# Performance work log

Hardware: AMD Instinct MI355X
Metric: run time of the kernel (lower is better)

Reference implementation:

```python
import jax, jax.numpy as jnp
import numpy as np

B, S, D, H = 2, 2048, 1024, 16
DK = D // H

def setup_inputs() -> dict:
    key = jax.random.key(0)
    ks = jax.random.split(key, 12)
    def lin(k, shape, fan_in):
        bound = 1.0 / np.sqrt(fan_in)
        return jax.random.uniform(k, shape, jnp.float32, -bound, bound)
    inp = {
        'Q': jax.random.normal(ks[0], (B, S, D), jnp.float32),
        'K': jax.random.normal(ks[1], (B, S, D), jnp.float32),
        'V': jax.random.normal(ks[2], (B, S, D), jnp.float32),
        # padding mask: last 128 key positions of batch element 0 are padding
        'padding_mask': jnp.ones((B, 1, 1, S), jnp.int32).at[0, :, :, -128:].set(0),
        # causal look-ahead mask
        'look_ahead_mask': jnp.tril(jnp.ones((S, S), jnp.int32))[None, None],
        'Wq': lin(ks[3], (D, D), D), 'bq': lin(ks[4], (D,), D),
        'Wk': lin(ks[5], (D, D), D), 'bk': lin(ks[6], (D,), D),
        'Wv': lin(ks[7], (D, D), D), 'bv': lin(ks[8], (D,), D),
        'Wo': lin(ks[9], (D, D), D), 'bo': lin(ks[10], (D,), D),
    }
    return inp

def _split_heads(x):
    # [B,S,D] -> [B,H,S,DK]
    b, s, _ = x.shape
    return x.reshape(b, s, H, DK).transpose(0, 2, 1, 3)

def reference(Q, K, V, padding_mask, look_ahead_mask, Wq, bq, Wk, bk, Wv, bv, Wo, bo):
    q = _split_heads(Q @ Wq.T + bq)  # [B,H,S,DK]
    k = _split_heads(K @ Wk.T + bk)
    v = _split_heads(V @ Wv.T + bv)
    scores = jnp.einsum('bhqd,bhkd->bhqk', q, k) / np.sqrt(DK).astype(np.float32)
    neg_inf = jnp.float32(-jnp.inf)
    scores = jnp.where(padding_mask == 0, neg_inf, scores)
    scores = jnp.where(look_ahead_mask == 0, neg_inf, scores)
    weights = jax.nn.softmax(scores, axis=-1)  # dropout is identity in eval mode
    x = jnp.einsum('bhqk,bhkd->bhqd', weights, v)  # [B,H,S,DK]
    x = x.transpose(0, 2, 1, 3).reshape(Q.shape[0], Q.shape[1], D)
    return x @ Wo.T + bo
```

## Files before the change

kernel.cpp:

```cpp
#include <hip/hip_runtime.h>
#include <hip/hip_bf16.h>

#define B_   2
#define S_   2048
#define D_   1024
#define H_   16
#define DK_  64

typedef unsigned short u16;
typedef __attribute__((ext_vector_type(8))) short bf16x8;
typedef __attribute__((ext_vector_type(4))) float f32x4;

#define QSCALE   0.18033688011112042f
#define SMBIAS  -8.656170245333781f

static __device__ __forceinline__ u16 f2bf(float f) {
  union { float f; unsigned u; } v; v.f = f;
  unsigned r = v.u + 0x7FFF + ((v.u >> 16) & 1);
  return (u16)(r >> 16);
}

static __device__ __forceinline__ void gl_lds16(const void* g, void* l) {
  __builtin_amdgcn_global_load_lds(
      (const __attribute__((address_space(1))) void*)g,
      (__attribute__((address_space(3))) void*)l, 16, 0, 0);
}

__global__ void cvt3(const float4* __restrict__ a, const float4* __restrict__ b, const float4* __restrict__ c,
                     ushort4* __restrict__ oa, ushort4* __restrict__ ob, ushort4* __restrict__ oc, int n4) {
  int y = blockIdx.y;
  const float4* in = (y == 0) ? a : (y == 1) ? b : c;
  ushort4* out = (y == 0) ? oa : (y == 1) ? ob : oc;
  int i = blockIdx.x * blockDim.x + threadIdx.x;
  if (i < n4) {
    float4 v = in[i];
    ushort4 r;
    r.x = f2bf(v.x); r.y = f2bf(v.y); r.z = f2bf(v.z); r.w = f2bf(v.w);
    out[i] = r;
  }
}
__global__ void cvt4(const float4* __restrict__ a, const float4* __restrict__ b, const float4* __restrict__ c,
                     const float4* __restrict__ d, ushort4* __restrict__ oa, ushort4* __restrict__ ob,
                     ushort4* __restrict__ oc, ushort4* __restrict__ od, int n4) {
  int y = blockIdx.y;
  const float4* in = (y == 0) ? a : (y == 1) ? b : (y == 2) ? c : d;
  ushort4* out = (y == 0) ? oa : (y == 1) ? ob : (y == 2) ? oc : od;
  int i = blockIdx.x * blockDim.x + threadIdx.x;
  if (i < n4) {
    float4 v = in[i];
    ushort4 r;
    r.x = f2bf(v.x); r.y = f2bf(v.y); r.z = f2bf(v.z); r.w = f2bf(v.w);
    out[i] = r;
  }
}

__launch_bounds__(256, 2)
__global__ void gemm_qkv(const u16* __restrict__ Xq, const u16* __restrict__ Xk, const u16* __restrict__ Xv,
                         const u16* __restrict__ Wq, const u16* __restrict__ Wk, const u16* __restrict__ Wv,
                         const float* __restrict__ bq, const float* __restrict__ bk, const float* __restrict__ bv,
                         u16* __restrict__ outq, u16* __restrict__ outk, u16* __restrict__ outv) {
  const int z = blockIdx.z;
  const u16* Am; const u16* Bm; int m0, n0;
  if (z == 2) { Am = Wv; Bm = Xv; m0 = blockIdx.x * 128; n0 = blockIdx.y * 128; }
  else if (z == 1) { Am = Xk; Bm = Wk; m0 = blockIdx.y * 128; n0 = blockIdx.x * 128; }
  else { Am = Xq; Bm = Wq; m0 = blockIdx.y * 128; n0 = blockIdx.x * 128; }
  const float* bias = (z == 0) ? bq : (z == 1) ? bk : bv;

  __shared__ __align__(16) u16 As[2][128 * 32];
  __shared__ __align__(16) u16 Bs[2][128 * 32];

  const int tid = threadIdx.x, lane = tid & 63, w = tid >> 6;
  const int q = lane >> 4, cl = lane & 15;
  const int wr = w >> 1, wc = w & 1;

#pragma unroll
  for (int i = 0; i < 2; ++i) {
    int cb = (i * 4 + w) * 64;
    int ch = cb + lane;
    int row = ch >> 2, ko = (ch & 3) << 3;
    gl_lds16(Am + (size_t)(m0 + row) * D_ + ko, As[0] + cb * 8);
    gl_lds16(Bm + (size_t)(n0 + row) * D_ + ko, Bs[0] + cb * 8);
  }

  f32x4 acc[4][4] = {};

  for (int it = 0; it < 32; ++it) {
    const int buf = it & 1;
    __syncthreads();

    if (it < 31) {
      const int k0 = (it + 1) * 32;
#pragma unroll
      for (int i = 0; i < 2; ++i) {
        int cb = (i * 4 + w) * 64;
        int ch = cb + lane;
        int row = ch >> 2, ko = (ch & 3) << 3;
        gl_lds16(Am + (size_t)(m0 + row) * D_ + k0 + ko, As[buf ^ 1] + cb * 8);
        gl_lds16(Bm + (size_t)(n0 + row) * D_ + k0 + ko, Bs[buf ^ 1] + cb * 8);
      }
    }

    const u16* At = As[buf];
    const u16* Bt = Bs[buf];
    bf16x8 af[4], bfr[4];
#pragma unroll
    for (int r = 0; r < 4; ++r) af[r]  = *(const bf16x8*)(At + (wr * 64 + r * 16 + cl) * 32 + q * 8);
#pragma unroll
    for (int c = 0; c < 4; ++c) bfr[c] = *(const bf16x8*)(Bt + (wc * 64 + c * 16 + cl) * 32 + q * 8);
#pragma unroll
    for (int r = 0; r < 4; ++r)
#pragma unroll
      for (int c = 0; c < 4; ++c)
        acc[r][c] = __builtin_amdgcn_mfma_f32_16x16x32_bf16(af[r], bfr[c], acc[r][c], 0, 0, 0);
  }

  if (z == 2) {
#pragma unroll
    for (int r = 0; r < 4; ++r) {
#pragma unroll
      for (int rr = 0; rr < 4; ++rr) {
        int j = m0 + wr * 64 + r * 16 + q * 4 + rr;
        float bval = bias[j];
        int hh = j >> 6, dk = j & 63;
#pragma unroll
        for (int c = 0; c < 4; ++c) {
          int n = n0 + wc * 64 + c * 16 + cl;
          int bb = n >> 11, s = n & (S_ - 1);
          outv[((size_t)(bb * H_ + hh) * DK_ + dk) * S_ + s] = f2bf(acc[r][c][rr] + bval);
        }
      }
    }
  } else {
    const float scale = (z == 0) ? QSCALE : 1.0f;
    u16* o = (z == 0) ? outq : outk;
#pragma unroll
    for (int c = 0; c < 4; ++c) {
      int j = n0 + wc * 64 + c * 16 + cl;
      float bval = bias[j];
      int hh = j >> 6, dk = j & 63;
#pragma unroll
      for (int r = 0; r < 4; ++r) {
#pragma unroll
        for (int rr = 0; rr < 4; ++rr) {
          int n = m0 + wr * 64 + r * 16 + q * 4 + rr;
          int bb = n >> 11, s = n & (S_ - 1);
          o[((size_t)(bb * H_ + hh) * S_ + s) * DK_ + dk] = f2bf((acc[r][c][rr] + bval) * scale);
        }
      }
    }
  }
}

__launch_bounds__(256, 2)
__global__ void attn(const u16* __restrict__ qh, const u16* __restrict__ kh,
                     const u16* __restrict__ vt, const int* __restrict__ pad,
                     u16* __restrict__ attn_out) {
  __shared__ __align__(16) u16 Ks[2][64 * 64];
  __shared__ __align__(16) u16 Vs[2][64 * 64];
  __shared__ __align__(16) u16 Ps[4][16 * 72];

  const int tid = threadIdx.x, lane = tid & 63, w = tid >> 6;
  const int q = lane >> 4, cl = lane & 15;
  const int qt = (int)gridDim.x - 1 - (int)blockIdx.x;
  const int qb = qt * 64, h = blockIdx.y, b = blockIdx.z;

  const u16* Q = qh + (size_t)(b * H_ + h) * S_ * DK_;
  const u16* K = kh + (size_t)(b * H_ + h) * S_ * DK_;
  const u16* V = vt + (size_t)(b * H_ + h) * DK_ * S_;
  const int* pm = pad + b * S_;

  const int qr0 = qb + w * 16;
  bf16x8 qf0 = *(const bf16x8*)(Q + (qr0 + cl) * DK_ + q * 8);
  bf16x8 qf1 = *(const bf16x8*)(Q + (qr0 + cl) * DK_ + 32 + q * 8);

  f32x4 o[4] = {};
  float ls[4] = {0.f, 0.f, 0.f, 0.f};
  u16* Pw = Ps[w];

  const int nkv = qt + 1;

#pragma unroll
  for (int i = 0; i < 2; ++i) {
    int s = (i * 4 + w) * 64 + lane;
    int row = s >> 3;
    int c = (s & 7) ^ (row & 7);
    gl_lds16(K + (size_t)row * DK_ + (c << 3), Ks[0] + (size_t)s * 8);
    gl_lds16(V + (size_t)row * S_ + (c << 3), Vs[0] + (size_t)s * 8);
  }

  for (int it = 0; it < nkv; ++it) {
    const int kb = it << 6;
    const int buf = it & 1;
    __syncthreads();

    if (it + 1 < nkv) {
      const int kb2 = (it + 1) << 6;
#pragma unroll
      for (int i = 0; i < 2; ++i) {
        int s = (i * 4 + w) * 64 + lane;
        int row = s >> 3;
        int c = (s & 7) ^ (row & 7);
        gl_lds16(K + (size_t)(kb2 + row) * DK_ + (c << 3), Ks[buf ^ 1] + (size_t)s * 8);
        gl_lds16(V + (size_t)row * S_ + kb2 + (c << 3), Vs[buf ^ 1] + (size_t)s * 8);
      }
    }

    const u16* Kt = Ks[buf];
    const u16* Vt = Vs[buf];

    bf16x8 kf[4][2];
#pragma unroll
    for (int ct = 0; ct < 4; ++ct) {
      int rk = ct * 16 + cl;
      int c0 = q ^ (rk & 7);
      kf[ct][0] = *(const bf16x8*)(Kt + rk * 64 + (c0 << 3));
      kf[ct][1] = *(const bf16x8*)(Kt + rk * 64 + ((c0 ^ 4) << 3));
    }

    float kbv[4];
#pragma unroll
    for (int ct = 0; ct < 4; ++ct)
      kbv[ct] = (pm[kb + ct * 16 + cl] != 0) ? SMBIAS : -3e38f;

    f32x4 sa[4];
#pragma unroll
    for (int ct = 0; ct < 4; ++ct) {
      f32x4 zz = {};
      zz = __builtin_amdgcn_mfma_f32_16x16x32_bf16(qf0, kf[ct][0], zz, 0, 0, 0);
      zz = __builtin_amdgcn_mfma_f32_16x16x32_bf16(qf1, kf[ct][1], zz, 0, 0, 0);
      sa[ct] = zz;
    }

    if (it < qt) {
#pragma unroll
      for (int ct = 0; ct < 4; ++ct)
#pragma unroll
        for (int rr = 0; rr < 4; ++rr) {
          float p = exp2f(sa[ct][rr] + kbv[ct]);
          ls[rr] += p;
          Pw[(q * 4 + rr) * 72 + ct * 16 + cl] = f2bf(p);
        }
    } else {
#pragma unroll
      for (int ct = 0; ct < 4; ++ct) {
        int kg = kb + ct * 16 + cl;
#pragma unroll
        for (int rr = 0; rr < 4; ++rr) {
          int qg = qr0 + q * 4 + rr;
          float p = (kg <= qg) ? exp2f(sa[ct][rr] + kbv[ct]) : 0.f;
          ls[rr] += p;
          Pw[(q * 4 + rr) * 72 + ct * 16 + cl] = f2bf(p);
        }
      }
    }

    bf16x8 pf0 = *(const bf16x8*)(Pw + cl * 72 + q * 8);
    bf16x8 pf1 = *(const bf16x8*)(Pw + cl * 72 + 32 + q * 8);

#pragma unroll
    for (int ct = 0; ct < 4; ++ct) {
      int rv = ct * 16 + cl;
      int c0 = q ^ (rv & 7);
      bf16x8 vf0 = *(const bf16x8*)(Vt + rv * 64 + (c0 << 3));
      bf16x8 vf1 = *(const bf16x8*)(Vt + rv * 64 + ((c0 ^ 4) << 3));
      o[ct] = __builtin_amdgcn_mfma_f32_16x16x32_bf16(pf0, vf0, o[ct], 0, 0, 0);
      o[ct] = __builtin_amdgcn_mfma_f32_16x16x32_bf16(pf1, vf1, o[ct], 0, 0, 0);
    }
  }

#pragma unroll
  for (int rr = 0; rr < 4; ++rr) {
    float l = ls[rr];
    l += __shfl_xor(l, 1, 64);
    l += __shfl_xor(l, 2, 64);
    l += __shfl_xor(l, 4, 64);
    l += __shfl_xor(l, 8, 64);
    float inv = 1.0f / l;
    int qg = qr0 + q * 4 + rr;
    size_t base = (size_t)(b * S_ + qg) * D_ + h * DK_;
#pragma unroll
    for (int ct = 0; ct < 4; ++ct)
      attn_out[base + ct * 16 + cl] = f2bf(o[ct][rr] * inv);
  }
}

__launch_bounds__(256, 2)
__global__ void gemm_out(const u16* __restrict__ A, const u16* __restrict__ W,
                         const float* __restrict__ bias, float* __restrict__ out) {
  __shared__ __align__(16) u16 As[2][128 * 32];
  __shared__ __align__(16) u16 Bs[2][64 * 32];

  const int tid = threadIdx.x, lane = tid & 63, w = tid >> 6;
  const int q = lane >> 4, cl = lane & 15;
  const int m0 = blockIdx.y * 128, n0 = blockIdx.x * 64;

#pragma unroll
  for (int i = 0; i < 2; ++i) {
    int cb = (i * 4 + w) * 64;
    int ch = cb + lane;
    int row = ch >> 2, ko = (ch & 3) << 3;
    gl_lds16(A + (size_t)(m0 + row) * D_ + ko, As[0] + cb * 8);
  }
  {
    int cb = w * 64;
    int ch = cb + lane;
    int row = ch >> 2, ko = (ch & 3) << 3;
    gl_lds16(W + (size_t)(n0 + row) * D_ + ko, Bs[0] + cb * 8);
  }

  f32x4 acc[2][4] = {};

  for (int it = 0; it < 32; ++it) {
    const int buf = it & 1;
    __syncthreads();

    if (it < 31) {
      const int k0 = (it + 1) * 32;
#pragma unroll
      for (int i = 0; i < 2; ++i) {
        int cb = (i * 4 + w) * 64;
        int ch = cb + lane;
        int row = ch >> 2, ko = (ch & 3) << 3;
        gl_lds16(A + (size_t)(m0 + row) * D_ + k0 + ko, As[buf ^ 1] + cb * 8);
      }
      {
        int cb = w * 64;
        int ch = cb + lane;
        int row = ch >> 2, ko = (ch & 3) << 3;
        gl_lds16(W + (size_t)(n0 + row) * D_ + k0 + ko, Bs[buf ^ 1] + cb * 8);
      }
    }

    const u16* At = As[buf];
    const u16* Bt = Bs[buf];
    bf16x8 af[2], bfr[4];
#pragma unroll
    for (int r = 0; r < 2; ++r) af[r]  = *(const bf16x8*)(At + (w * 32 + r * 16 + cl) * 32 + q * 8);
#pragma unroll
    for (int c = 0; c < 4; ++c) bfr[c] = *(const bf16x8*)(Bt + (c * 16 + cl) * 32 + q * 8);
#pragma unroll
    for (int r = 0; r < 2; ++r)
#pragma unroll
      for (int c = 0; c < 4; ++c)
        acc[r][c] = __builtin_amdgcn_mfma_f32_16x16x32_bf16(af[r], bfr[c], acc[r][c], 0, 0, 0);
  }

#pragma unroll
  for (int c = 0; c < 4; ++c) {
    int j = n0 + c * 16 + cl;
    float bval = bias[j];
#pragma unroll
    for (int r = 0; r < 2; ++r) {
#pragma unroll
      for (int rr = 0; rr < 4; ++rr) {
        int n = m0 + w * 32 + r * 16 + q * 4 + rr;
        out[(size_t)n * D_ + j] = acc[r][c][rr] + bval;
      }
    }
  }
}

extern "C" void kernel_launch(void* const* d_in, const int* in_sizes, int n_in,
                              void* d_out, int out_size, void* d_ws, size_t ws_size,
                              hipStream_t stream) {
  const float* Qf  = (const float*)d_in[0];
  const float* Kf  = (const float*)d_in[1];
  const float* Vf  = (const float*)d_in[2];
  const int*   pad = (const int*)d_in[3];
  const float* Wqf = (const float*)d_in[5];
  const float* bq  = (const float*)d_in[6];
  const float* Wkf = (const float*)d_in[7];
  const float* bk  = (const float*)d_in[8];
  const float* Wvf = (const float*)d_in[9];
  const float* bv  = (const float*)d_in[10];
  const float* Wof = (const float*)d_in[11];
  const float* bo  = (const float*)d_in[12];

  const size_t BSD = (size_t)B_ * S_ * D_;
  const size_t DD  = (size_t)D_ * D_;

  char* ws = (char*)d_ws;
  u16* Qb   = (u16*)ws; ws += BSD * 2;
  u16* Kb   = (u16*)ws; ws += BSD * 2;
  u16* Vb   = (u16*)ws; ws += BSD * 2;
  u16* Wqb  = (u16*)ws; ws += DD * 2;
  u16* Wkb  = (u16*)ws; ws += DD * 2;
  u16* Wvb  = (u16*)ws; ws += DD * 2;
  u16* Wob  = (u16*)ws; ws += DD * 2;
  u16* qhd  = (u16*)ws; ws += BSD * 2;
  u16* khd  = (u16*)ws; ws += BSD * 2;
  u16* vtd  = (u16*)ws; ws += BSD * 2;
  u16* attn_o = (u16*)ws; ws += BSD * 2;

  const int n4 = (int)(BSD / 4);
  const int w4 = (int)(DD / 4);
  dim3 gc3(n4 / 256, 3), gc4(w4 / 256, 4);
  cvt3<<<gc3, 256, 0, stream>>>((const float4*)Qf, (const float4*)Kf, (const float4*)Vf,
                                (ushort4*)Qb, (ushort4*)Kb, (ushort4*)Vb, n4);
  cvt4<<<gc4, 256, 0, stream>>>((const float4*)Wqf, (const float4*)Wkf, (const float4*)Wvf, (const float4*)Wof,
                                (ushort4*)Wqb, (ushort4*)Wkb, (ushort4*)Wvb, (ushort4*)Wob, w4);

  dim3 g1(D_ / 128, (B_ * S_) / 128, 3);
  gemm_qkv<<<g1, 256, 0, stream>>>(Qb, Kb, Vb, Wqb, Wkb, Wvb, bq, bk, bv, qhd, khd, vtd);

  dim3 g2(S_ / 64, H_, B_);
  attn<<<g2, 256, 0, stream>>>(qhd, khd, vtd, pad, attn_o);

  dim3 g3(D_ / 64, (B_ * S_) / 128);
  gemm_out<<<g3, 256, 0, stream>>>(attn_o, Wob, bo, (float*)d_out);
}
```

Baseline: 288.6 us.

## Load attention K/V fragments directly from global memory and merge conversion kernels

The attention kernel no longer stages K and V tiles through double-buffered LDS with async global-to-LDS copies and block barriers. Each wave now reads its K and V MFMA fragments straight from global memory, relying on L2/L1 caching, and interleaves the score MFMAs with the softmax per column tile. Launch bounds are raised to 4 blocks per SIMD to hide the added global latency with occupancy. The two fp32-to-bf16 conversion kernels are merged into one launch, which over-provisions blocks for the small weight matrices. The trade is that each of the four waves in a block now fetches the same K/V tile separately, so the kernel becomes more dependent on cache hit rates.

Result: slower. 420.9 us (+45.8%).

```diff
diff --git a/kernel.cpp b/kernel.cpp
--- a/kernel.cpp
+++ b/kernel.cpp
@@ -26,27 +26,27 @@
       (__attribute__((address_space(3))) void*)l, 16, 0, 0);
 }
 
-__global__ void cvt3(const float4* __restrict__ a, const float4* __restrict__ b, const float4* __restrict__ c,
-                     ushort4* __restrict__ oa, ushort4* __restrict__ ob, ushort4* __restrict__ oc, int n4) {
+__global__ void cvt_all(const float4* __restrict__ s0, const float4* __restrict__ s1,
+                        const float4* __restrict__ s2, const float4* __restrict__ s3,
+                        const float4* __restrict__ s4, const float4* __restrict__ s5,
+                        const float4* __restrict__ s6,
+                        ushort4* __restrict__ d0, ushort4* __restrict__ d1,
+                        ushort4* __restrict__ d2, ushort4* __restrict__ d3,
+                        ushort4* __restrict__ d4, ushort4* __restrict__ d5,
+                        ushort4* __restrict__ d6, int nbig, int nsmall) {
   int y = blockIdx.y;
-  const float4* in = (y == 0) ? a : (y == 1) ? b : c;
-  ushort4* out = (y == 0) ? oa : (y == 1) ? ob : oc;
+  const float4* in; ushort4* out; int n;
+  switch (y) {
+    case 0: in = s0; out = d0; n = nbig; break;
+    case 1: in = s1; out = d1; n = nbig; break;
+    case 2: in = s2; out = d2; n = nbig; break;
+    case 3: in = s3; out = d3; n = nsmall; break;
+    case 4: in = s4; out = d4; n = nsmall; break;
+    case 5: in = s5; out = d5; n = nsmall; break;
+    default: in = s6; out = d6; n = nsmall; break;
+  }
   int i = blockIdx.x * blockDim.x + threadIdx.x;
-  if (i < n4) {
-    float4 v = in[i];
-    ushort4 r;
-    r.x = f2bf(v.x); r.y = f2bf(v.y); r.z = f2bf(v.z); r.w = f2bf(v.w);
-    out[i] = r;
-  }
-}
-__global__ void cvt4(const float4* __restrict__ a, const float4* __restrict__ b, const float4* __restrict__ c,
-                     const float4* __restrict__ d, ushort4* __restrict__ oa, ushort4* __restrict__ ob,
-                     ushort4* __restrict__ oc, ushort4* __restrict__ od, int n4) {
-  int y = blockIdx.y;
-  const float4* in = (y == 0) ? a : (y == 1) ? b : (y == 2) ? c : d;
-  ushort4* out = (y == 0) ? oa : (y == 1) ? ob : (y == 2) ? oc : od;
-  int i = blockIdx.x * blockDim.x + threadIdx.x;
-  if (i < n4) {
+  if (i < n) {
     float4 v = in[i];
     ushort4 r;
     r.x = f2bf(v.x); r.y = f2bf(v.y); r.z = f2bf(v.z); r.w = f2bf(v.w);
@@ -151,12 +151,10 @@
   }
 }
 
-__launch_bounds__(256, 2)
+__launch_bounds__(256, 4)
 __global__ void attn(const u16* __restrict__ qh, const u16* __restrict__ kh,
                      const u16* __restrict__ vt, const int* __restrict__ pad,
                      u16* __restrict__ attn_out) {
-  __shared__ __align__(16) u16 Ks[2][64 * 64];
-  __shared__ __align__(16) u16 Vs[2][64 * 64];
   __shared__ __align__(16) u16 Ps[4][16 * 72];
 
   const int tid = threadIdx.x, lane = tid & 63, w = tid >> 6;
@@ -178,43 +176,15 @@
   u16* Pw = Ps[w];
 
   const int nkv = qt + 1;
-
-#pragma unroll
-  for (int i = 0; i < 2; ++i) {
-    int s = (i * 4 + w) * 64 + lane;
-    int row = s >> 3;
-    int c = (s & 7) ^ (row & 7);
-    gl_lds16(K + (size_t)row * DK_ + (c << 3), Ks[0] + (size_t)s * 8);
-    gl_lds16(V + (size_t)row * S_ + (c << 3), Vs[0] + (size_t)s * 8);
-  }
-
   for (int it = 0; it < nkv; ++it) {
     const int kb = it << 6;
-    const int buf = it & 1;
-    __syncthreads();
-
-    if (it + 1 < nkv) {
-      const int kb2 = (it + 1) << 6;
-#pragma unroll
-      for (int i = 0; i < 2; ++i) {
-        int s = (i * 4 + w) * 64 + lane;
-        int row = s >> 3;
-        int c = (s & 7) ^ (row & 7);
-        gl_lds16(K + (size_t)(kb2 + row) * DK_ + (c << 3), Ks[buf ^ 1] + (size_t)s * 8);
-        gl_lds16(V + (size_t)row * S_ + kb2 + (c << 3), Vs[buf ^ 1] + (size_t)s * 8);
-      }
-    }
-
-    const u16* Kt = Ks[buf];
-    const u16* Vt = Vs[buf];
-
-    bf16x8 kf[4][2];
+
+    bf16x8 vf[4][2];
 #pragma unroll
     for (int ct = 0; ct < 4; ++ct) {
-      int rk = ct * 16 + cl;
-      int c0 = q ^ (rk & 7);
-      kf[ct][0] = *(const bf16x8*)(Kt + rk * 64 + (c0 << 3));
-      kf[ct][1] = *(const bf16x8*)(Kt + rk * 64 + ((c0 ^ 4) << 3));
+      const u16* vrow = V + (size_t)(ct * 16 + cl) * S_ + kb;
+      vf[ct][0] = *(const bf16x8*)(vrow + q * 8);
+      vf[ct][1] = *(const bf16x8*)(vrow + 32 + q * 8);
     }
 
     float kbv[4];
@@ -222,32 +192,36 @@
     for (int ct = 0; ct < 4; ++ct)
       kbv[ct] = (pm[kb + ct * 16 + cl] != 0) ? SMBIAS : -3e38f;
 
-    f32x4 sa[4];
-#pragma unroll
-    for (int ct = 0; ct < 4; ++ct) {
-      f32x4 zz = {};
-      zz = __builtin_amdgcn_mfma_f32_16x16x32_bf16(qf0, kf[ct][0], zz, 0, 0, 0);
-      zz = __builtin_amdgcn_mfma_f32_16x16x32_bf16(qf1, kf[ct][1], zz, 0, 0, 0);
-      sa[ct] = zz;
-    }
-
     if (it < qt) {
 #pragma unroll
-      for (int ct = 0; ct < 4; ++ct)
+      for (int ct = 0; ct < 4; ++ct) {
+        const u16* krow = K + (size_t)(kb + ct * 16 + cl) * DK_;
+        bf16x8 kf0 = *(const bf16x8*)(krow + q * 8);
+        bf16x8 kf1 = *(const bf16x8*)(krow + 32 + q * 8);
+        f32x4 zz = {};
+        zz = __builtin_amdgcn_mfma_f32_16x16x32_bf16(qf0, kf0, zz, 0, 0, 0);
+        zz = __builtin_amdgcn_mfma_f32_16x16x32_bf16(qf1, kf1, zz, 0, 0, 0);
 #pragma unroll
         for (int rr = 0; rr < 4; ++rr) {
-          float p = exp2f(sa[ct][rr] + kbv[ct]);
+          float p = exp2f(zz[rr] + kbv[ct]);
           ls[rr] += p;
           Pw[(q * 4 + rr) * 72 + ct * 16 + cl] = f2bf(p);
         }
+      }
     } else {
 #pragma unroll
       for (int ct = 0; ct < 4; ++ct) {
+        const u16* krow = K + (size_t)(kb + ct * 16 + cl) * DK_;
+        bf16x8 kf0 = *(const bf16x8*)(krow + q * 8);
+        bf16x8 kf1 = *(const bf16x8*)(krow + 32 + q * 8);
+        f32x4 zz = {};
+        zz = __builtin_amdgcn_mfma_f32_16x16x32_bf16(qf0, kf0, zz, 0, 0, 0);
+        zz = __builtin_amdgcn_mfma_f32_16x16x32_bf16(qf1, kf1, zz, 0, 0, 0);
         int kg = kb + ct * 16 + cl;
 #pragma unroll
         for (int rr = 0; rr < 4; ++rr) {
           int qg = qr0 + q * 4 + rr;
-          float p = (kg <= qg) ? exp2f(sa[ct][rr] + kbv[ct]) : 0.f;
+          float p = (kg <= qg) ? exp2f(zz[rr] + kbv[ct]) : 0.f;
           ls[rr] += p;
           Pw[(q * 4 + rr) * 72 + ct * 16 + cl] = f2bf(p);
         }
@@ -259,12 +233,8 @@
 
 #pragma unroll
     for (int ct = 0; ct < 4; ++ct) {
-      int rv = ct * 16 + cl;
-      int c0 = q ^ (rv & 7);
-      bf16x8 vf0 = *(const bf16x8*)(Vt + rv * 64 + (c0 << 3));
-      bf16x8 vf1 = *(const bf16x8*)(Vt + rv * 64 + ((c0 ^ 4) << 3));
-      o[ct] = __builtin_amdgcn_mfma_f32_16x16x32_bf16(pf0, vf0, o[ct], 0, 0, 0);
-      o[ct] = __builtin_amdgcn_mfma_f32_16x16x32_bf16(pf1, vf1, o[ct], 0, 0, 0);
+      o[ct] = __builtin_amdgcn_mfma_f32_16x16x32_bf16(pf0, vf[ct][0], o[ct], 0, 0, 0);
+      o[ct] = __builtin_amdgcn_mfma_f32_16x16x32_bf16(pf1, vf[ct][1], o[ct], 0, 0, 0);
     }
   }
 
@@ -394,11 +364,12 @@
 
   const int n4 = (int)(BSD / 4);
   const int w4 = (int)(DD / 4);
-  dim3 gc3(n4 / 256, 3), gc4(w4 / 256, 4);
-  cvt3<<<gc3, 256, 0, stream>>>((const float4*)Qf, (const float4*)Kf, (const float4*)Vf,
-                                (ushort4*)Qb, (ushort4*)Kb, (ushort4*)Vb, n4);
-  cvt4<<<gc4, 256, 0, stream>>>((const float4*)Wqf, (const float4*)Wkf, (const float4*)Wvf, (const float4*)Wof,
-                                (ushort4*)Wqb, (ushort4*)Wkb, (ushort4*)Wvb, (ushort4*)Wob, w4);
+  dim3 gc(n4 / 256, 7);
+  cvt_all<<<gc, 256, 0, stream>>>((const float4*)Qf, (const float4*)Kf, (const float4*)Vf,
+                                  (const float4*)Wqf, (const float4*)Wkf, (const float4*)Wvf, (const float4*)Wof,
+                                  (ushort4*)Qb, (ushort4*)Kb, (ushort4*)Vb,
+                                  (ushort4*)Wqb, (ushort4*)Wkb, (ushort4*)Wvb, (ushort4*)Wob,
+                                  n4, w4);
 
   dim3 g1(D_ / 128, (B_ * S_) / 128, 3);
   gemm_qkv<<<g1, 256, 0, stream>>>(Qb, Kb, Vb, Wqb, Wkb, Wvb, bq, bk, bv, qhd, khd, vtd);
```
